# Kernel optimization log

Hardware: AMD Instinct MI355X
Metric: run time of the kernel (lower is better)

The kernel has to match this reference:

```python
import jax, jax.numpy as jnp
import numpy as np
from jax import lax

LOOKBACK = 48
HORIZON = 12
INPUT_DIM = 8
OUTPUT_DIM = 1
HIDDEN = 128
NUM_LAYERS = 2
BG_IDX = 0
BATCH = 8192


def _lstm_cell(x, h, c, W_ih, W_hh, b_ih, b_hh):
    # x:[B,Din] h,c:[B,H]; PyTorch gate order i,f,g,o
    g = x @ W_ih.T + h @ W_hh.T + b_ih + b_hh
    i, f, gg, o = jnp.split(g, 4, axis=-1)
    c_new = jax.nn.sigmoid(f) * c + jax.nn.sigmoid(i) * jnp.tanh(gg)
    h_new = jax.nn.sigmoid(o) * jnp.tanh(c_new)
    return h_new, c_new


def setup_inputs() -> dict:
    key = jax.random.key(0)
    ks = jax.random.split(key, 16)
    k_scale = 1.0 / np.sqrt(HIDDEN)
    u = lambda k, shp: jax.random.uniform(k, shp, jnp.float32, -k_scale, k_scale)
    inp = {
        "inputs": jax.random.normal(ks[0], (BATCH, LOOKBACK + HORIZON, INPUT_DIM), jnp.float32),
        "W_ih_0": u(ks[1], (4 * HIDDEN, INPUT_DIM)),
        "W_hh_0": u(ks[2], (4 * HIDDEN, HIDDEN)),
        "b_ih_0": u(ks[3], (4 * HIDDEN,)),
        "b_hh_0": u(ks[4], (4 * HIDDEN,)),
        "W_ih_1": u(ks[5], (4 * HIDDEN, HIDDEN)),
        "W_hh_1": u(ks[6], (4 * HIDDEN, HIDDEN)),
        "b_ih_1": u(ks[7], (4 * HIDDEN,)),
        "b_hh_1": u(ks[8], (4 * HIDDEN,)),
        "W_fc": u(ks[9], (OUTPUT_DIM, HIDDEN)),
        "b_fc": u(ks[10], (OUTPUT_DIM,)),
    }
    return inp


def _forward(inputs, params, W_fc, b_fc):
    B = inputs.shape[0]
    # ---- encode lookback window, layer by layer (time-major scan) ----
    xs = jnp.swapaxes(inputs[:, :LOOKBACK, :], 0, 1)  # [T,B,D]
    finals_h, finals_c = [], []
    for (Wi, Wh, bi, bh) in params:
        h0 = jnp.zeros((B, HIDDEN), inputs.dtype)
        c0 = jnp.zeros((B, HIDDEN), inputs.dtype)
        def cell(carry, x, Wi=Wi, Wh=Wh, bi=bi, bh=bh):
            h, c = carry
            h, c = _lstm_cell(x, h, c, Wi, Wh, bi, bh)
            return (h, c), h
        (hT, cT), xs = lax.scan(cell, (h0, c0), xs)
        finals_h.append(hT)
        finals_c.append(cT)
    hs0 = jnp.stack(finals_h)  # [L,B,H]
    cs0 = jnp.stack(finals_c)

    dec_xs = jnp.swapaxes(inputs[:, LOOKBACK:, :], 0, 1)  # [Th,B,D]
    ts = jnp.arange(HORIZON)

    def step(carry, inp):
        hs, cs, last_bg = carry
        x, t = inp
        bg = jnp.where(t > 0, last_bg, x[:, BG_IDX])
        x = x.at[:, BG_IDX].set(bg)
        new_hs, new_cs = [], []
        cur = x
        for l, (Wi, Wh, bi, bh) in enumerate(params):
            h, c = _lstm_cell(cur, hs[l], cs[l], Wi, Wh, bi, bh)
            new_hs.append(h)
            new_cs.append(c)
            cur = h
        pred = cur @ W_fc.T + b_fc  # [B,O]
        return (jnp.stack(new_hs), jnp.stack(new_cs), pred[:, 0]), pred

    init = (hs0, cs0, jnp.zeros((B,), inputs.dtype))
    _, preds = lax.scan(step, init, (dec_xs, ts))  # [Th,B,O]
    return jnp.swapaxes(preds, 0, 1)  # [B,Th,O]


def reference(inputs, W_ih_0, W_hh_0, b_ih_0, b_hh_0, W_ih_1, W_hh_1, b_ih_1, b_hh_1, W_fc, b_fc):
    params = [(W_ih_0, W_hh_0, b_ih_0, b_hh_0), (W_ih_1, W_hh_1, b_ih_1, b_hh_1)]
    return _forward(inputs, params, W_fc, b_fc)
```

## Files before the change

### kernel.cpp

```cpp
#include <hip/hip_runtime.h>

#define LOOKBACK 48
#define HORIZON  12
#define TTOT     60
#define INPUT_DIM 8
#define HIDDEN   128
#define GATES    512
#define BATCH    8192
#define TILE_B   32
#define NTHREADS 512
#define NSLICES  8
#define L0_KS    5
#define L1_KS    8
#define FRAGS_PER_KS 4
#define FRAG_SHORTS 512
#define KSTRIDE  (FRAGS_PER_KS * FRAG_SHORTS)
#define SLICE_FRAGS ((L0_KS + L1_KS) * FRAGS_PER_KS)
#define W_HALFS  (NSLICES * SLICE_FRAGS * FRAG_SHORTS)

#define ROWP 33
#define A0_CHUNKS 20
#define A1_CHUNKS 16
#define A0_HALFS (A0_CHUNKS * ROWP * 8)
#define A1_HALFS (A1_CHUNKS * ROWP * 8)

typedef __attribute__((ext_vector_type(8))) _Float16 half8;
typedef __attribute__((ext_vector_type(4))) float f32x4;

__device__ __forceinline__ float frcp(float x) { return __builtin_amdgcn_rcpf(x); }

__device__ __forceinline__ float sigm(float x) {
    return frcp(1.0f + __expf(-x));
}
__device__ __forceinline__ float tanh_fast(float x) {
    float ax = fabsf(x);
    float e  = __expf(-2.0f * ax);
    float t  = (1.0f - e) * frcp(1.0f + e);
    return copysignf(t, x);
}

#define BARRIER() __asm__ volatile("s_waitcnt lgkmcnt(0)\ns_barrier" ::: "memory")

__global__ void setup_kernel(const float* __restrict__ Wih0, const float* __restrict__ Whh0,
                             const float* __restrict__ bi0,  const float* __restrict__ bh0,
                             const float* __restrict__ Wih1, const float* __restrict__ Whh1,
                             const float* __restrict__ bi1,  const float* __restrict__ bh1,
                             _Float16* __restrict__ wfrag, float* __restrict__ bias) {
    int idx = blockIdx.x * blockDim.x + threadIdx.x;
    if (idx < W_HALFS) {
        int e = idx & 511, frag = idx >> 9;
        int lane = e >> 3, j = e & 7;
        int t = frag & 3;
        int rest = frag >> 2;
        int lks = rest % (L0_KS + L1_KS), s = rest / (L0_KS + L1_KS);
        int l = (lks < L0_KS) ? 0 : 1;
        int ks = l ? (lks - L0_KS) : lks;
        int k = ks * 32 + ((lane >> 4) << 3) + j;
        int uu = s * 16 + (lane & 15);
        int row = t * HIDDEN + uu;
        float v = 0.0f;
        if (l == 0) {
            if (k < INPUT_DIM) v = Wih0[row * INPUT_DIM + k];
            else if (k < INPUT_DIM + HIDDEN) v = Whh0[row * HIDDEN + (k - INPUT_DIM)];
        } else {
            if (k < HIDDEN) v = Wih1[row * HIDDEN + k];
            else v = Whh1[row * HIDDEN + (k - HIDDEN)];
        }
        wfrag[idx] = (_Float16)v;
    } else if (idx < W_HALFS + 2 * GATES) {
        int g = idx - W_HALFS;
        bias[g] = (g < GATES) ? (bi0[g] + bh0[g]) : (bi1[g - GATES] + bh1[g - GATES]);
    }
}

__global__ __launch_bounds__(NTHREADS, 2)
void lstm_kernel(const float* __restrict__ input,
                 const _Float16* __restrict__ wfrag,
                 const float* __restrict__ bias01,
                 const float* __restrict__ W_fc,
                 const float* __restrict__ b_fc,
                 float* __restrict__ out) {
    __shared__ _Float16 A0[A0_HALFS];
    __shared__ _Float16 A1[A1_HALFS];
    __shared__ float wfcs[HIDDEN];

    const int tid  = threadIdx.x;
    const int lane = tid & 63;
    const int s    = tid >> 6;
    const int col  = lane & 15;
    const int quad = lane >> 4;
    const int u    = s * 16 + col;
    const int batch0 = blockIdx.x * TILE_B;

    const _Float16* w0 = wfrag + s * (SLICE_FRAGS * FRAG_SHORTS);
    const _Float16* w1 = w0 + L0_KS * KSTRIDE;

    for (int i = tid; i < A0_HALFS; i += NTHREADS) A0[i] = (_Float16)0.f;
    for (int i = tid; i < A1_HALFS; i += NTHREADS) A1[i] = (_Float16)0.f;
    if (tid < HIDDEN) wfcs[tid] = W_fc[tid];
    const float bfc = b_fc[0];

    float bv0[4], bv1[4];
#pragma unroll
    for (int tt = 0; tt < 4; ++tt) {
        bv0[tt] = bias01[tt * HIDDEN + u];
        bv1[tt] = bias01[GATES + tt * HIDDEN + u];
    }

    float c0[2][4] = {}, c1[2][4] = {};

    float xv = 0.0f;
    if (tid < TILE_B * INPUT_DIM)
        xv = input[(size_t)(batch0 + (tid >> 3)) * (TTOT * INPUT_DIM) + (tid & 7)];
    BARRIER();
    if (tid < TILE_B * INPUT_DIM)
        A0[(tid >> 3) * 8 + (tid & 7)] = (_Float16)xv;

    half8 bq[3][4];
    half8 ah[2][2];

#define WPOS(p) ((p) < L0_KS ? (w0 + (p) * KSTRIDE) : (w1 + ((p) - L0_KS) * KSTRIDE))
#define LOADB(p, sl) { const _Float16* wp_ = WPOS(p) + lane * 8;                \
    _Pragma("unroll") for (int tt = 0; tt < 4; ++tt)                            \
        bq[sl][tt] = *(const half8*)(wp_ + tt * FRAG_SHORTS); }
#define LOADA(H, chunk, buf) { int base_ = ((chunk) * ROWP + col) * 8;          \
    ah[buf][0] = *(const half8*)(H + base_);                                    \
    ah[buf][1] = *(const half8*)(H + base_ + 16 * 8); }
#define COMP(ACC, ab, sl)                                                       \
    _Pragma("unroll") for (int tt = 0; tt < 4; ++tt)                            \
    _Pragma("unroll") for (int mt = 0; mt < 2; ++mt)                            \
        ACC[mt][tt] = __builtin_amdgcn_mfma_f32_16x16x32_f16(                   \
            ah[ab][mt], bq[sl][tt], ACC[mt][tt], 0, 0, 0);

    LOADB(0, 0) LOADB(1, 1) LOADB(2, 2)
    BARRIER();

#pragma unroll 1
    for (int t = 0; t < TTOT; ++t) {
        if (tid < TILE_B * INPUT_DIM && t + 1 < TTOT)
            xv = input[(size_t)(batch0 + (tid >> 3)) * (TTOT * INPUT_DIM)
                       + (t + 1) * INPUT_DIM + (tid & 7)];

        f32x4 acc[2][4];
#pragma unroll
        for (int tt = 0; tt < 4; ++tt) {
            f32x4 b = {bv0[tt], bv0[tt], bv0[tt], bv0[tt]};
            acc[0][tt] = b; acc[1][tt] = b;
        }
        LOADA(A0, quad, 0)
        LOADA(A0, 4 + quad, 1)  COMP(acc, 0, 0) LOADB(3, 0)
        LOADA(A0, 8 + quad, 0)  COMP(acc, 1, 1) LOADB(4, 1)
        LOADA(A0, 12 + quad, 1) COMP(acc, 0, 2) LOADB(5, 2)
        LOADA(A0, 16 + quad, 0) COMP(acc, 1, 0) LOADB(6, 0)
                                COMP(acc, 0, 1) LOADB(7, 1)
        BARRIER();

#pragma unroll
        for (int mt = 0; mt < 2; ++mt) {
#pragma unroll
            for (int r = 0; r < 4; ++r) {
                float ig = sigm(acc[mt][0][r]);
                float fg = sigm(acc[mt][1][r]);
                float gg = tanh_fast(acc[mt][2][r]);
                float og = sigm(acc[mt][3][r]);
                float cn = fg * c0[mt][r] + ig * gg;
                c0[mt][r] = cn;
                float h = og * tanh_fast(cn);
                int row = mt * 16 + quad * 4 + r;
                A0[((1 + (u >> 3)) * ROWP + row) * 8 + (u & 7)] = (_Float16)h;
            }
        }
        if (tid < TILE_B * INPUT_DIM && t + 1 < TTOT) {
            int r = tid >> 3, k = tid & 7;
            if (!(t + 1 > LOOKBACK && k == 0))
                A0[r * 8 + k] = (_Float16)xv;
        }
        BARRIER();

#pragma unroll
        for (int tt = 0; tt < 4; ++tt) {
            f32x4 b = {bv1[tt], bv1[tt], bv1[tt], bv1[tt]};
            acc[0][tt] = b; acc[1][tt] = b;
        }
        LOADA(A0, 1 + quad, 0)
        LOADA(A0, 5 + quad, 1)   COMP(acc, 0, 2) LOADB(8, 2)
        LOADA(A0, 9 + quad, 0)   COMP(acc, 1, 0) LOADB(9, 0)
        LOADA(A0, 13 + quad, 1)  COMP(acc, 0, 1) LOADB(10, 1)
        LOADA(A1, quad, 0)       COMP(acc, 1, 2) LOADB(11, 2)
        LOADA(A1, 4 + quad, 1)   COMP(acc, 0, 0) LOADB(12, 0)
        LOADA(A1, 8 + quad, 0)   COMP(acc, 1, 1) LOADB(1, 1)
        LOADA(A1, 12 + quad, 1)  COMP(acc, 0, 2) LOADB(2, 2)
                                 COMP(acc, 1, 0) LOADB(0, 0)
        BARRIER();

#pragma unroll
        for (int mt = 0; mt < 2; ++mt) {
#pragma unroll
            for (int r = 0; r < 4; ++r) {
                float ig = sigm(acc[mt][0][r]);
                float fg = sigm(acc[mt][1][r]);
                float gg = tanh_fast(acc[mt][2][r]);
                float og = sigm(acc[mt][3][r]);
                float cn = fg * c1[mt][r] + ig * gg;
                c1[mt][r] = cn;
                float h = og * tanh_fast(cn);
                int row = mt * 16 + quad * 4 + r;
                A1[((u >> 3) * ROWP + row) * 8 + (u & 7)] = (_Float16)h;
            }
        }

        if (t >= LOOKBACK) {
            BARRIER();
            int r = tid >> 4, sub = tid & 15;
            float p = 0.0f;
#pragma unroll
            for (int i = 0; i < HIDDEN / 16; ++i) {
                int uu = sub + i * 16;
                p += (float)A1[((uu >> 3) * ROWP + r) * 8 + (uu & 7)] * wfcs[uu];
            }
#pragma unroll
            for (int off = 8; off; off >>= 1) p += __shfl_down(p, off, 16);
            if (sub == 0) {
                float pr = p + bfc;
                out[(size_t)(batch0 + r) * HORIZON + (t - LOOKBACK)] = pr;
                if (t + 1 < TTOT)
                    A0[r * 8] = (_Float16)pr;
            }
            BARRIER();
        }
    }
#undef WPOS
#undef LOADB
#undef LOADA
#undef COMP
}

extern "C" void kernel_launch(void* const* d_in, const int* in_sizes, int n_in,
                              void* d_out, int out_size, void* d_ws, size_t ws_size,
                              hipStream_t stream) {
    const float* input = (const float*)d_in[0];
    const float* Wih0  = (const float*)d_in[1];
    const float* Whh0  = (const float*)d_in[2];
    const float* bi0   = (const float*)d_in[3];
    const float* bh0   = (const float*)d_in[4];
    const float* Wih1  = (const float*)d_in[5];
    const float* Whh1  = (const float*)d_in[6];
    const float* bi1   = (const float*)d_in[7];
    const float* bh1   = (const float*)d_in[8];
    const float* W_fc  = (const float*)d_in[9];
    const float* b_fc  = (const float*)d_in[10];

    _Float16* wfrag = (_Float16*)d_ws;
    float* bias = (float*)((char*)d_ws + (size_t)W_HALFS * sizeof(_Float16));

    int total = W_HALFS + 2 * GATES;
    setup_kernel<<<(total + 255) / 256, 256, 0, stream>>>(
        Wih0, Whh0, bi0, bh0, Wih1, Whh1, bi1, bh1, wfrag, bias);

    lstm_kernel<<<BATCH / TILE_B, NTHREADS, 0, stream>>>(
        input, wfrag, bias, W_fc, b_fc, (float*)d_out);
}
```

Measured before the change: 411.3 us.

## Double-buffer LDS hidden-state tiles to drop two barriers per timestep

Doubles the A0/A1 LDS hidden/input buffers and ping-pongs between them by timestep parity. Reads and writes now go to different buffers, which removes the barriers after each layer's MFMA phase and leaves one barrier between layers per step. It also makes the weight base pointer wave-uniform with readfirstlane so weight loads can use scalar addressing. The cost is twice the LDS footprint, which may reduce occupancy, plus the burden of getting the cross-step read/write hazard ordering right.

```diff
diff --git a/kernel.cpp b/kernel.cpp
--- a/kernel.cpp
+++ b/kernel.cpp
@@ -21,14 +21,15 @@
 #define ROWP 33
 #define A0_CHUNKS 20
 #define A1_CHUNKS 16
-#define A0_HALFS (A0_CHUNKS * ROWP * 8)
-#define A1_HALFS (A1_CHUNKS * ROWP * 8)
+#define A0_BUF (A0_CHUNKS * ROWP * 8)
+#define A1_BUF (A1_CHUNKS * ROWP * 8)
+#define A0_HALFS (2 * A0_BUF)
+#define A1_HALFS (2 * A1_BUF)
 
 typedef __attribute__((ext_vector_type(8))) _Float16 half8;
 typedef __attribute__((ext_vector_type(4))) float f32x4;
 
 __device__ __forceinline__ float frcp(float x) { return __builtin_amdgcn_rcpf(x); }
-
 __device__ __forceinline__ float sigm(float x) {
     return frcp(1.0f + __expf(-x));
 }
@@ -92,8 +93,10 @@
     const int u    = s * 16 + col;
     const int batch0 = blockIdx.x * TILE_B;
 
-    const _Float16* w0 = wfrag + s * (SLICE_FRAGS * FRAG_SHORTS);
-    const _Float16* w1 = w0 + L0_KS * KSTRIDE;
+    uintptr_t wp64 = (uintptr_t)(wfrag + s * (SLICE_FRAGS * FRAG_SHORTS));
+    wp64 = ((uintptr_t)__builtin_amdgcn_readfirstlane((unsigned)(wp64 >> 32)) << 32)
+         | __builtin_amdgcn_readfirstlane((unsigned)wp64);
+    const _Float16* wbase = (const _Float16*)wp64;
 
     for (int i = tid; i < A0_HALFS; i += NTHREADS) A0[i] = (_Float16)0.f;
     for (int i = tid; i < A1_HALFS; i += NTHREADS) A1[i] = (_Float16)0.f;
@@ -119,11 +122,11 @@
     half8 bq[3][4];
     half8 ah[2][2];
 
-#define WPOS(p) ((p) < L0_KS ? (w0 + (p) * KSTRIDE) : (w1 + ((p) - L0_KS) * KSTRIDE))
-#define LOADB(p, sl) { const _Float16* wp_ = WPOS(p) + lane * 8;                \
+#define LOADB(p, sl) {                                                          \
     _Pragma("unroll") for (int tt = 0; tt < 4; ++tt)                            \
-        bq[sl][tt] = *(const half8*)(wp_ + tt * FRAG_SHORTS); }
-#define LOADA(H, chunk, buf) { int base_ = ((chunk) * ROWP + col) * 8;          \
+        bq[sl][tt] = *(const half8*)(wbase + (p) * KSTRIDE                      \
+                                     + tt * FRAG_SHORTS + lane * 8); }
+#define LOADA(H, off, chunk, buf) { int base_ = (off) + ((chunk) * ROWP + col) * 8; \
     ah[buf][0] = *(const half8*)(H + base_);                                    \
     ah[buf][1] = *(const half8*)(H + base_ + 16 * 8); }
 #define COMP(ACC, ab, sl)                                                       \
@@ -137,6 +140,10 @@
 
 #pragma unroll 1
     for (int t = 0; t < TTOT; ++t) {
+        const int rb = t & 1, wb = rb ^ 1;
+        const int a0r = rb * A0_BUF, a0w = wb * A0_BUF;
+        const int a1r = rb * A1_BUF, a1w = wb * A1_BUF;
+
         if (tid < TILE_B * INPUT_DIM && t + 1 < TTOT)
             xv = input[(size_t)(batch0 + (tid >> 3)) * (TTOT * INPUT_DIM)
                        + (t + 1) * INPUT_DIM + (tid & 7)];
@@ -147,13 +154,12 @@
             f32x4 b = {bv0[tt], bv0[tt], bv0[tt], bv0[tt]};
             acc[0][tt] = b; acc[1][tt] = b;
         }
-        LOADA(A0, quad, 0)
-        LOADA(A0, 4 + quad, 1)  COMP(acc, 0, 0) LOADB(3, 0)
-        LOADA(A0, 8 + quad, 0)  COMP(acc, 1, 1) LOADB(4, 1)
-        LOADA(A0, 12 + quad, 1) COMP(acc, 0, 2) LOADB(5, 2)
-        LOADA(A0, 16 + quad, 0) COMP(acc, 1, 0) LOADB(6, 0)
-                                COMP(acc, 0, 1) LOADB(7, 1)
-        BARRIER();
+        LOADA(A0, a0r, quad, 0)
+        LOADA(A0, a0r, 4 + quad, 1)  COMP(acc, 0, 0) LOADB(3, 0)
+        LOADA(A0, a0r, 8 + quad, 0)  COMP(acc, 1, 1) LOADB(4, 1)
+        LOADA(A0, a0r, 12 + quad, 1) COMP(acc, 0, 2) LOADB(5, 2)
+        LOADA(A0, a0r, 16 + quad, 0) COMP(acc, 1, 0) LOADB(6, 0)
+                                     COMP(acc, 0, 1) LOADB(7, 1)
 
 #pragma unroll
         for (int mt = 0; mt < 2; ++mt) {
@@ -167,13 +173,13 @@
                 c0[mt][r] = cn;
                 float h = og * tanh_fast(cn);
                 int row = mt * 16 + quad * 4 + r;
-                A0[((1 + (u >> 3)) * ROWP + row) * 8 + (u & 7)] = (_Float16)h;
+                A0[a0w + ((1 + (u >> 3)) * ROWP + row) * 8 + (u & 7)] = (_Float16)h;
             }
         }
         if (tid < TILE_B * INPUT_DIM && t + 1 < TTOT) {
             int r = tid >> 3, k = tid & 7;
             if (!(t + 1 > LOOKBACK && k == 0))
-                A0[r * 8 + k] = (_Float16)xv;
+                A0[a0w + r * 8 + k] = (_Float16)xv;
         }
         BARRIER();
 
@@ -182,16 +188,15 @@
             f32x4 b = {bv1[tt], bv1[tt], bv1[tt], bv1[tt]};
             acc[0][tt] = b; acc[1][tt] = b;
         }
-        LOADA(A0, 1 + quad, 0)
-        LOADA(A0, 5 + quad, 1)   COMP(acc, 0, 2) LOADB(8, 2)
-        LOADA(A0, 9 + quad, 0)   COMP(acc, 1, 0) LOADB(9, 0)
-        LOADA(A0, 13 + quad, 1)  COMP(acc, 0, 1) LOADB(10, 1)
-        LOADA(A1, quad, 0)       COMP(acc, 1, 2) LOADB(11, 2)
-        LOADA(A1, 4 + quad, 1)   COMP(acc, 0, 0) LOADB(12, 0)
-        LOADA(A1, 8 + quad, 0)   COMP(acc, 1, 1) LOADB(1, 1)
-        LOADA(A1, 12 + quad, 1)  COMP(acc, 0, 2) LOADB(2, 2)
-                                 COMP(acc, 1, 0) LOADB(0, 0)
-        BARRIER();
+        LOADA(A0, a0w, 1 + quad, 0)
+        LOADA(A0, a0w, 5 + quad, 1)   COMP(acc, 0, 2) LOADB(8, 2)
+        LOADA(A0, a0w, 9 + quad, 0)   COMP(acc, 1, 0) LOADB(9, 0)
+        LOADA(A0, a0w, 13 + quad, 1)  COMP(acc, 0, 1) LOADB(10, 1)
+        LOADA(A1, a1r, quad, 0)       COMP(acc, 1, 2) LOADB(11, 2)
+        LOADA(A1, a1r, 4 + quad, 1)   COMP(acc, 0, 0) LOADB(12, 0)
+        LOADA(A1, a1r, 8 + quad, 0)   COMP(acc, 1, 1) LOADB(1, 1)
+        LOADA(A1, a1r, 12 + quad, 1)  COMP(acc, 0, 2) LOADB(2, 2)
+                                      COMP(acc, 1, 0) LOADB(0, 0)
 
 #pragma unroll
         for (int mt = 0; mt < 2; ++mt) {
@@ -205,7 +210,7 @@
                 c1[mt][r] = cn;
                 float h = og * tanh_fast(cn);
                 int row = mt * 16 + quad * 4 + r;
-                A1[((u >> 3) * ROWP + row) * 8 + (u & 7)] = (_Float16)h;
+                A1[a1w + ((u >> 3) * ROWP + row) * 8 + (u & 7)] = (_Float16)h;
             }
         }
 
@@ -216,7 +221,7 @@
 #pragma unroll
             for (int i = 0; i < HIDDEN / 16; ++i) {
                 int uu = sub + i * 16;
-                p += (float)A1[((uu >> 3) * ROWP + r) * 8 + (uu & 7)] * wfcs[uu];
+                p += (float)A1[a1w + ((uu >> 3) * ROWP + r) * 8 + (uu & 7)] * wfcs[uu];
             }
 #pragma unroll
             for (int off = 8; off; off >>= 1) p += __shfl_down(p, off, 16);
@@ -224,12 +229,11 @@
                 float pr = p + bfc;
                 out[(size_t)(batch0 + r) * HORIZON + (t - LOOKBACK)] = pr;
                 if (t + 1 < TTOT)
-                    A0[r * 8] = (_Float16)pr;
+                    A0[a0w + r * 8] = (_Float16)pr;
             }
             BARRIER();
         }
     }
-#undef WPOS
 #undef LOADB
 #undef LOADA
 #undef COMP
```

Result: faster. 374.5 us (-8.9%).
